# Optimization experiments

Hardware: AMD Instinct MI355X
Metric: run time of the kernel (lower is better)

The kernel has to match this reference:

```python
import jax, jax.numpy as jnp
import numpy as np

N_NODES = 100000
N_EDGES = 1600000
IN_DIM = 64
HID = 128
N_ASSETS = 50
N_GRAPHS = 64


def setup_inputs() -> dict:
    key = jax.random.key(0)
    ks = jax.random.split(key, 12)
    x = jax.random.normal(ks[0], (N_NODES, IN_DIM), dtype=jnp.float32)
    edge_index = jax.random.randint(ks[1], (2, N_EDGES), 0, N_NODES, dtype=jnp.int64)
    batch = jnp.sort(jax.random.randint(ks[2], (N_NODES,), 0, N_GRAPHS, dtype=jnp.int64))
    def lin(k, fan_in, fan_out):
        bound = 1.0 / np.sqrt(fan_in)
        return jax.random.uniform(k, (fan_in, fan_out), jnp.float32, -bound, bound)
    return {
        "x": x,
        "edge_index": edge_index,
        "batch": batch,
        # GraphConv 1: lin_rel (with bias) on aggregated messages, lin_root (no bias)
        "w1_rel": lin(ks[3], IN_DIM, HID),
        "b1": jnp.zeros((HID,), jnp.float32),
        "w1_root": lin(ks[4], IN_DIM, HID),
        # GraphConv 2
        "w2_rel": lin(ks[5], HID, HID),
        "b2": jnp.zeros((HID,), jnp.float32),
        "w2_root": lin(ks[6], HID, HID),
        # MLP head
        "fc1_w": lin(ks[7], HID, HID),
        "fc1_b": jnp.zeros((HID,), jnp.float32),
        "fc2_w": lin(ks[8], HID, N_ASSETS),
        "fc2_b": jnp.zeros((N_ASSETS,), jnp.float32),
    }


def graph_conv(x, src, dst, w_rel, w_root, b):
    # out_i = W_rel @ (sum_{j: j->i} x_j) + W_root @ x_i + b  (PyG GraphConv, aggr='add')
    # Project first (cheaper traffic when out_dim <= in_dim is not guaranteed, but
    # aggregating raw features then projecting matches math; project-then-scatter is
    # equivalent by linearity and lets the scatter run at out width. Keep faithful
    # order: aggregate raw x_j, then lin_rel.
    agg = jax.ops.segment_sum(x[src], dst, num_segments=N_NODES)  # [N, in_dim]
    return agg @ w_rel + x @ w_root + b


def reference(x, edge_index, batch, w1_rel, b1, w1_root, w2_rel, b2, w2_root,
              fc1_w, fc1_b, fc2_w, fc2_b):
    src, dst = edge_index[0], edge_index[1]
    h = jax.nn.relu(graph_conv(x, src, dst, w1_rel, w1_root, b1))   # [N, HID]
    h = jax.nn.relu(graph_conv(h, src, dst, w2_rel, w2_root, b2))   # [N, HID]
    # global_mean_pool over batch segment ids
    sums = jax.ops.segment_sum(h, batch, num_segments=N_GRAPHS)     # [G, HID]
    cnts = jax.ops.segment_sum(jnp.ones((h.shape[0], 1), h.dtype), batch,
                               num_segments=N_GRAPHS)               # [G, 1]
    pooled = sums / jnp.maximum(cnts, 1.0)
    out = jax.nn.relu(pooled @ fc1_w + fc1_b)
    logits = out @ fc2_w + fc2_b
    return jax.nn.softmax(logits, axis=-1)
```

## Files before the change

kernel.cpp:

```cpp
#include <hip/hip_runtime.h>
#include <math.h>

#define N_NODES_C 100000
#define N_EDGES_C 1600000
#define IN_DIM_C 64
#define HID_C 128
#define N_ASSETS_C 50
#define N_GRAPHS_C 64

#define BKT_SHIFT 9
#define BKT_NODES 512
#define NB_BKT ((N_NODES_C + BKT_NODES - 1) / BKT_NODES)
#define EPB_A 8192
#define NBLK_A ((N_EDGES_C + EPB_A - 1) / EPB_A)

typedef __attribute__((ext_vector_type(8))) short bf16x8;
typedef __attribute__((ext_vector_type(4))) float f32x4;

__device__ __forceinline__ unsigned short f2bf(float f) {
    unsigned u = __float_as_uint(f);
    return (unsigned short)((u + 0x7FFFu + ((u >> 16) & 1u)) >> 16);
}
__device__ __forceinline__ float bf2f(unsigned short b) {
    return __uint_as_float((unsigned)b << 16);
}

__global__ __launch_bounds__(256) void cast_bf16_kernel(
    const float* __restrict__ src, unsigned short* __restrict__ dst, int n4)
{
    int i = blockIdx.x * 256 + threadIdx.x;
    if (i < n4) {
        float4 v = ((const float4*)src)[i];
        ushort4 o;
        o.x = f2bf(v.x); o.y = f2bf(v.y); o.z = f2bf(v.z); o.w = f2bf(v.w);
        ((ushort4*)dst)[i] = o;
    }
}

__global__ __launch_bounds__(64) void pack_w_kernel(
    const float* __restrict__ W, unsigned short* __restrict__ dst)
{
    int kc = blockIdx.x >> 3;
    int ct = blockIdx.x & 7;
    int lane = threadIdx.x;
    int quad = lane >> 4;
    int l16 = lane & 15;
    unsigned short hi[8], lo[8];
#pragma unroll
    for (int j = 0; j < 8; ++j) {
        float w = W[(size_t)(kc * 32 + quad * 8 + j) * HID_C + ct * 16 + l16];
        unsigned short h = f2bf(w);
        float r = w - bf2f(h);
        hi[j] = h;
        lo[j] = f2bf(r);
    }
    size_t base = ((size_t)(kc * 8 + ct) * 2) * 512 + (size_t)lane * 8;
#pragma unroll
    for (int j = 0; j < 8; ++j) {
        dst[base + j] = hi[j];
        dst[base + 512 + j] = lo[j];
    }
}

__global__ __launch_bounds__(256) void bucket_hist_kernel(
    const int* __restrict__ ei, int* __restrict__ bcnt)
{
    __shared__ int cnt[NB_BKT];
    int t = threadIdx.x;
    for (int i = t; i < NB_BKT; i += 256) cnt[i] = 0;
    __syncthreads();
    int base = blockIdx.x * 2048;
#pragma unroll
    for (int i = 0; i < 8; ++i) {
        int e = base + i * 256 + t;
        if (e < N_EDGES_C) {
            int dst = ei[N_EDGES_C + e];
            atomicAdd(&cnt[dst >> BKT_SHIFT], 1);
        }
    }
    __syncthreads();
    for (int i = t; i < NB_BKT; i += 256)
        if (cnt[i]) atomicAdd(&bcnt[i], cnt[i]);
}

__global__ __launch_bounds__(256) void bucket_scan_kernel(
    const int* __restrict__ bcnt, int* __restrict__ bbase, int* __restrict__ gcur)
{
    __shared__ int s[256];
    int t = threadIdx.x;
    int v = (t < NB_BKT) ? bcnt[t] : 0;
    s[t] = v;
    __syncthreads();
    for (int o = 1; o < 256; o <<= 1) {
        int x = (t >= o) ? s[t - o] : 0;
        __syncthreads();
        s[t] += x;
        __syncthreads();
    }
    int excl = s[t] - v;
    if (t < NB_BKT) { bbase[t] = excl; gcur[t] = excl; }
    if (t == 255) bbase[NB_BKT] = s[255];
}

__global__ __launch_bounds__(256) void partition_kernel(
    const int* __restrict__ ei, int* __restrict__ gcur,
    unsigned* __restrict__ tmp)
{
    __shared__ unsigned stage[EPB_A];
    __shared__ unsigned stage2[EPB_A];
    __shared__ unsigned char sbkt[EPB_A];
    __shared__ unsigned char sbkt2[EPB_A];
    __shared__ int cnt[NB_BKT];
    __shared__ int base[NB_BKT];
    __shared__ int cur[NB_BKT];
    __shared__ int gb[NB_BKT];
    __shared__ int s[256];

    const int t = threadIdx.x;
    const int e0 = blockIdx.x * EPB_A;
    const int nE = min(EPB_A, N_EDGES_C - e0);

    for (int i = t; i < NB_BKT; i += 256) cnt[i] = 0;
    __syncthreads();

    for (int idx = t; idx < nE; idx += 256) {
        int e = e0 + idx;
        int src = ei[e];
        int dst = ei[N_EDGES_C + e];
        int b = dst >> BKT_SHIFT;
        stage[idx] = ((unsigned)(dst & (BKT_NODES - 1)) << 17) | (unsigned)src;
        sbkt[idx] = (unsigned char)b;
        atomicAdd(&cnt[b], 1);
    }
    __syncthreads();

    int v = (t < NB_BKT) ? cnt[t] : 0;
    s[t] = v;
    __syncthreads();
    for (int o = 1; o < 256; o <<= 1) {
        int x = (t >= o) ? s[t - o] : 0;
        __syncthreads();
        s[t] += x;
        __syncthreads();
    }
    if (t < NB_BKT) {
        int excl = s[t] - v;
        base[t] = excl;
        cur[t] = excl;
        gb[t] = atomicAdd(&gcur[t], v);
    }
    __syncthreads();

    for (int idx = t; idx < nE; idx += 256) {
        int b = sbkt[idx];
        int p = atomicAdd(&cur[b], 1);
        stage2[p] = stage[idx];
        sbkt2[p] = (unsigned char)b;
    }
    __syncthreads();

    for (int idx = t; idx < nE; idx += 256) {
        int b = sbkt2[idx];
        int dest = gb[b] + (idx - base[b]);
        tmp[dest] = stage2[idx];
    }
}

__global__ __launch_bounds__(256) void bucket_sort_kernel(
    const unsigned* __restrict__ tmp, const int* __restrict__ bbase,
    int* __restrict__ row_ptr, int* __restrict__ col)
{
    __shared__ int ldeg[BKT_NODES];
    __shared__ int lsum[256];
    const int t = threadIdx.x;
    const int b = blockIdx.x;
    const int beg = bbase[b];
    const int end = bbase[b + 1];

    ldeg[t] = 0; ldeg[t + 256] = 0;
    __syncthreads();

    for (int p = beg + t; p < end; p += 256)
        atomicAdd(&ldeg[tmp[p] >> 17], 1);
    __syncthreads();

    int a0 = ldeg[2 * t], a1 = ldeg[2 * t + 1];
    int pair = a0 + a1;
    lsum[t] = pair;
    __syncthreads();
    for (int o = 1; o < 256; o <<= 1) {
        int x = (t >= o) ? lsum[t - o] : 0;
        __syncthreads();
        lsum[t] += x;
        __syncthreads();
    }
    int ep = lsum[t] - pair;
    __syncthreads();
    ldeg[2 * t] = ep;
    ldeg[2 * t + 1] = ep + a0;

    int gn0 = b * BKT_NODES + 2 * t;
    if (gn0 < N_NODES_C)     row_ptr[gn0] = beg + ep;
    if (gn0 + 1 < N_NODES_C) row_ptr[gn0 + 1] = beg + ep + a0;
    if (b == NB_BKT - 1 && t == 0) row_ptr[N_NODES_C] = N_EDGES_C;
    __syncthreads();

    for (int p = beg + t; p < end; p += 256) {
        unsigned v = tmp[p];
        int pos = atomicAdd(&ldeg[v >> 17], 1);
        col[beg + pos] = (int)(v & 0x1FFFFu);
    }
}

__global__ __launch_bounds__(256) void gather_bf128_kernel(
    const unsigned short* __restrict__ feat, const int* __restrict__ row_ptr,
    const int* __restrict__ col, unsigned short* __restrict__ agg)
{
    int wave = threadIdx.x >> 6;
    int lane = threadIdx.x & 63;
    int g = lane >> 4;
    int c = lane & 15;
    int n = blockIdx.x * 4 + wave;
    if (n >= N_NODES_C) return;
    int beg = row_ptr[n], end = row_ptr[n + 1];
    const uint4* f4 = (const uint4*)feat;

    float acc[8];
#pragma unroll
    for (int j = 0; j < 8; ++j) acc[j] = 0.f;

    int e = beg + g;
    for (; e + 4 < end; e += 8) {
        int s0 = col[e], s1 = col[e + 4];
        uint4 v0 = f4[(size_t)s0 * 16 + c];
        uint4 v1 = f4[(size_t)s1 * 16 + c];
        acc[0] += __uint_as_float(v0.x << 16) + __uint_as_float(v1.x << 16);
        acc[1] += __uint_as_float(v0.x & 0xFFFF0000u) + __uint_as_float(v1.x & 0xFFFF0000u);
        acc[2] += __uint_as_float(v0.y << 16) + __uint_as_float(v1.y << 16);
        acc[3] += __uint_as_float(v0.y & 0xFFFF0000u) + __uint_as_float(v1.y & 0xFFFF0000u);
        acc[4] += __uint_as_float(v0.z << 16) + __uint_as_float(v1.z << 16);
        acc[5] += __uint_as_float(v0.z & 0xFFFF0000u) + __uint_as_float(v1.z & 0xFFFF0000u);
        acc[6] += __uint_as_float(v0.w << 16) + __uint_as_float(v1.w << 16);
        acc[7] += __uint_as_float(v0.w & 0xFFFF0000u) + __uint_as_float(v1.w & 0xFFFF0000u);
    }
    if (e < end) {
        uint4 v = f4[(size_t)col[e] * 16 + c];
        acc[0] += __uint_as_float(v.x << 16);
        acc[1] += __uint_as_float(v.x & 0xFFFF0000u);
        acc[2] += __uint_as_float(v.y << 16);
        acc[3] += __uint_as_float(v.y & 0xFFFF0000u);
        acc[4] += __uint_as_float(v.z << 16);
        acc[5] += __uint_as_float(v.z & 0xFFFF0000u);
        acc[6] += __uint_as_float(v.w << 16);
        acc[7] += __uint_as_float(v.w & 0xFFFF0000u);
    }
#pragma unroll
    for (int j = 0; j < 8; ++j) {
        acc[j] += __shfl_xor(acc[j], 16, 64);
        acc[j] += __shfl_xor(acc[j], 32, 64);
    }
    if (g == 0) {
        uint4 o;
        o.x = (unsigned)f2bf(acc[0]) | ((unsigned)f2bf(acc[1]) << 16);
        o.y = (unsigned)f2bf(acc[2]) | ((unsigned)f2bf(acc[3]) << 16);
        o.z = (unsigned)f2bf(acc[4]) | ((unsigned)f2bf(acc[5]) << 16);
        o.w = (unsigned)f2bf(acc[6]) | ((unsigned)f2bf(acc[7]) << 16);
        ((uint4*)agg)[(size_t)n * 16 + c] = o;
    }
}

__global__ __launch_bounds__(256) void gather_bf64_kernel(
    const unsigned short* __restrict__ feat, const int* __restrict__ row_ptr,
    const int* __restrict__ col, unsigned short* __restrict__ agg)
{
    int wave = threadIdx.x >> 6;
    int lane = threadIdx.x & 63;
    int g = lane >> 3;
    int c = lane & 7;
    int n = blockIdx.x * 4 + wave;
    if (n >= N_NODES_C) return;
    int beg = row_ptr[n], end = row_ptr[n + 1];
    const uint4* f4 = (const uint4*)feat;

    float acc[8];
#pragma unroll
    for (int j = 0; j < 8; ++j) acc[j] = 0.f;

    int e = beg + g;
    for (; e + 8 < end; e += 16) {
        int s0 = col[e], s1 = col[e + 8];
        uint4 v0 = f4[(size_t)s0 * 8 + c];
        uint4 v1 = f4[(size_t)s1 * 8 + c];
        acc[0] += __uint_as_float(v0.x << 16) + __uint_as_float(v1.x << 16);
        acc[1] += __uint_as_float(v0.x & 0xFFFF0000u) + __uint_as_float(v1.x & 0xFFFF0000u);
        acc[2] += __uint_as_float(v0.y << 16) + __uint_as_float(v1.y << 16);
        acc[3] += __uint_as_float(v0.y & 0xFFFF0000u) + __uint_as_float(v1.y & 0xFFFF0000u);
        acc[4] += __uint_as_float(v0.z << 16) + __uint_as_float(v1.z << 16);
        acc[5] += __uint_as_float(v0.z & 0xFFFF0000u) + __uint_as_float(v1.z & 0xFFFF0000u);
        acc[6] += __uint_as_float(v0.w << 16) + __uint_as_float(v1.w << 16);
        acc[7] += __uint_as_float(v0.w & 0xFFFF0000u) + __uint_as_float(v1.w & 0xFFFF0000u);
    }
    if (e < end) {
        uint4 v = f4[(size_t)col[e] * 8 + c];
        acc[0] += __uint_as_float(v.x << 16);
        acc[1] += __uint_as_float(v.x & 0xFFFF0000u);
        acc[2] += __uint_as_float(v.y << 16);
        acc[3] += __uint_as_float(v.y & 0xFFFF0000u);
        acc[4] += __uint_as_float(v.z << 16);
        acc[5] += __uint_as_float(v.z & 0xFFFF0000u);
        acc[6] += __uint_as_float(v.w << 16);
        acc[7] += __uint_as_float(v.w & 0xFFFF0000u);
    }
#pragma unroll
    for (int j = 0; j < 8; ++j) {
        acc[j] += __shfl_xor(acc[j], 8, 64);
        acc[j] += __shfl_xor(acc[j], 16, 64);
        acc[j] += __shfl_xor(acc[j], 32, 64);
    }
    if (g == 0) {
        uint4 o;
        o.x = (unsigned)f2bf(acc[0]) | ((unsigned)f2bf(acc[1]) << 16);
        o.y = (unsigned)f2bf(acc[2]) | ((unsigned)f2bf(acc[3]) << 16);
        o.z = (unsigned)f2bf(acc[4]) | ((unsigned)f2bf(acc[5]) << 16);
        o.w = (unsigned)f2bf(acc[6]) | ((unsigned)f2bf(acc[7]) << 16);
        ((uint4*)agg)[(size_t)n * 8 + c] = o;
    }
}

template<int K>
__device__ __forceinline__ void conv_phase(
    const unsigned short* __restrict__ P, const unsigned short* __restrict__ WP,
    const int* rowIdx, int quad, int lane, int wv, f32x4 acc[4][2])
{
#pragma unroll
    for (int kc = 0; kc < K / 32; ++kc) {
        bf16x8 afr[4];
#pragma unroll
        for (int rt = 0; rt < 4; ++rt)
            afr[rt] = *(const bf16x8*)(P + (size_t)rowIdx[rt] * K + kc * 32 + quad * 8);
#pragma unroll
        for (int ci = 0; ci < 2; ++ci) {
            int ct = wv * 2 + ci;
            const unsigned short* bp = WP + ((size_t)(kc * 8 + ct) * 2) * 512 + (size_t)lane * 8;
            bf16x8 bhi = *(const bf16x8*)bp;
            bf16x8 blo = *(const bf16x8*)(bp + 512);
#pragma unroll
            for (int rt = 0; rt < 4; ++rt) {
                acc[rt][ci] = __builtin_amdgcn_mfma_f32_16x16x32_bf16(afr[rt], bhi, acc[rt][ci], 0, 0, 0);
                acc[rt][ci] = __builtin_amdgcn_mfma_f32_16x16x32_bf16(afr[rt], blo, acc[rt][ci], 0, 0, 0);
            }
        }
    }
}

template<int KA, int KX, bool OUTF32>
__global__ __launch_bounds__(256) void conv_mfma_kernel(
    const unsigned short* __restrict__ A, const unsigned short* __restrict__ X,
    const unsigned short* __restrict__ WrP, const unsigned short* __restrict__ WoP,
    const float* __restrict__ bias, void* __restrict__ outp, int N)
{
    const int t = threadIdx.x;
    const int wv = t >> 6;
    const int lane = t & 63;
    const int quad = lane >> 4;
    const int l16 = lane & 15;
    const int n0 = blockIdx.x * 64;

    f32x4 acc[4][2];
#pragma unroll
    for (int rt = 0; rt < 4; ++rt)
#pragma unroll
        for (int ci = 0; ci < 2; ++ci)
            acc[rt][ci] = (f32x4){0.f, 0.f, 0.f, 0.f};

    int rowIdx[4];
#pragma unroll
    for (int rt = 0; rt < 4; ++rt) {
        int r = n0 + rt * 16 + l16;
        rowIdx[rt] = (r < N) ? r : (N - 1);
    }

    conv_phase<KA>(A, WrP, rowIdx, quad, lane, wv, acc);
    conv_phase<KX>(X, WoP, rowIdx, quad, lane, wv, acc);

#pragma unroll
    for (int ci = 0; ci < 2; ++ci) {
        int colg = wv * 32 + ci * 16 + l16;
        float bv = bias[colg];
#pragma unroll
        for (int rt = 0; rt < 4; ++rt) {
            int nbase = n0 + rt * 16 + quad * 4;
#pragma unroll
            for (int r = 0; r < 4; ++r) {
                int node = nbase + r;
                if (node < N) {
                    float v = fmaxf(acc[rt][ci][r] + bv, 0.f);
                    if (OUTF32)
                        ((float*)outp)[(size_t)node * HID_C + colg] = v;
                    else
                        ((unsigned short*)outp)[(size_t)node * HID_C + colg] = f2bf(v);
                }
            }
        }
    }
}

__global__ __launch_bounds__(128) void pool_kernel(
    const float* __restrict__ h, const int* __restrict__ batch,
    float* __restrict__ pooled, float* __restrict__ cnts, int N)
{
    int j  = threadIdx.x;
    int n0 = blockIdx.x * 128;
    int nend = min(n0 + 128, N);
    int cur = -1;
    float sum = 0.f, cnt = 0.f;
    for (int n = n0; n < nend; ++n) {
        int g = batch[n];
        if (g != cur) {
            if (cur >= 0) {
                atomicAdd(&pooled[cur * HID_C + j], sum);
                if (j == 0) atomicAdd(&cnts[cur], cnt);
            }
            cur = g; sum = 0.f; cnt = 0.f;
        }
        sum += h[(size_t)n * HID_C + j];
        cnt += 1.f;
    }
    if (cur >= 0) {
        atomicAdd(&pooled[cur * HID_C + j], sum);
        if (j == 0) atomicAdd(&cnts[cur], cnt);
    }
}

__global__ __launch_bounds__(128) void head_kernel(
    const float* __restrict__ pooled, const float* __restrict__ cnts,
    const float* __restrict__ fc1w, const float* __restrict__ fc1b,
    const float* __restrict__ fc2w, const float* __restrict__ fc2b,
    float* __restrict__ out)
{
    __shared__ float sp[HID_C];
    __shared__ float so[HID_C];
    __shared__ float sl[64];
    __shared__ float sred[2];
    int g = blockIdx.x;
    int j = threadIdx.x;

    float inv = 1.f / fmaxf(cnts[g], 1.f);
    sp[j] = pooled[g * HID_C + j] * inv;
    __syncthreads();

    float a = fc1b[j];
    for (int k = 0; k < HID_C; ++k) a = fmaf(sp[k], fc1w[k * HID_C + j], a);
    so[j] = fmaxf(a, 0.f);
    __syncthreads();

    if (j < N_ASSETS_C) {
        float l = fc2b[j];
        for (int k = 0; k < HID_C; ++k) l = fmaf(so[k], fc2w[k * N_ASSETS_C + j], l);
        sl[j] = l;
    }
    __syncthreads();

    if (j == 0) {
        float m = -1e30f;
        for (int q = 0; q < N_ASSETS_C; ++q) m = fmaxf(m, sl[q]);
        sred[0] = m;
    }
    __syncthreads();
    if (j < N_ASSETS_C) sl[j] = expf(sl[j] - sred[0]);
    __syncthreads();
    if (j == 0) {
        float s = 0.f;
        for (int q = 0; q < N_ASSETS_C; ++q) s += sl[q];
        sred[1] = 1.f / s;
    }
    __syncthreads();
    if (j < N_ASSETS_C) out[g * N_ASSETS_C + j] = sl[j] * sred[1];
}

extern "C" void kernel_launch(void* const* d_in, const int* in_sizes, int n_in,
                              void* d_out, int out_size, void* d_ws, size_t ws_size,
                              hipStream_t stream)
{
    const float* x       = (const float*)d_in[0];
    const int*   ei      = (const int*)d_in[1];
    const int*   batch   = (const int*)d_in[2];
    const float* w1_rel  = (const float*)d_in[3];
    const float* b1      = (const float*)d_in[4];
    const float* w1_root = (const float*)d_in[5];
    const float* w2_rel  = (const float*)d_in[6];
    const float* b2      = (const float*)d_in[7];
    const float* w2_root = (const float*)d_in[8];
    const float* fc1w    = (const float*)d_in[9];
    const float* fc1b    = (const float*)d_in[10];
    const float* fc2w    = (const float*)d_in[11];
    const float* fc2b    = (const float*)d_in[12];
    float* out = (float*)d_out;

    char* ws = (char*)d_ws;
    unsigned*       tmp     = (unsigned*)(ws + 0);
    int*            col     = (int*)(ws + 6400000);
    int*            row_ptr = (int*)(ws + 12800000);
    int*            bcnt    = (int*)(ws + 13200016);
    int*            bbase   = (int*)(ws + 13200816);
    int*            gcur    = (int*)(ws + 13201616);
    unsigned short* wp1r    = (unsigned short*)(ws + 13202432);
    unsigned short* wp1o    = (unsigned short*)(ws + 13235200);
    unsigned short* wp2r    = (unsigned short*)(ws + 13267968);
    unsigned short* wp2o    = (unsigned short*)(ws + 13333504);
    float*          pooled  = (float*)(ws + 13399040);
    float*          cnts    = (float*)(ws + 13431808);
    unsigned short* xb      = (unsigned short*)(ws + 13432064);
    unsigned short* agg1b   = (unsigned short*)(ws + 26232064);
    unsigned short* h1b     = (unsigned short*)(ws + 39032064);
    unsigned short* agg2b   = (unsigned short*)(ws + 64632064);
    float*          h2      = (float*)(ws + 90232064);

    hipMemsetAsync(pooled, 0, 33024, stream);
    hipMemsetAsync(bcnt, 0, 800, stream);

    cast_bf16_kernel<<<(N_NODES_C * IN_DIM_C / 4 + 255) / 256, 256, 0, stream>>>(x, xb, N_NODES_C * IN_DIM_C / 4);
    pack_w_kernel<<<(IN_DIM_C / 32) * 8, 64, 0, stream>>>(w1_rel,  wp1r);
    pack_w_kernel<<<(IN_DIM_C / 32) * 8, 64, 0, stream>>>(w1_root, wp1o);
    pack_w_kernel<<<(HID_C  / 32) * 8, 64, 0, stream>>>(w2_rel,  wp2r);
    pack_w_kernel<<<(HID_C  / 32) * 8, 64, 0, stream>>>(w2_root, wp2o);

    bucket_hist_kernel<<<(N_EDGES_C + 2047) / 2048, 256, 0, stream>>>(ei, bcnt);
    bucket_scan_kernel<<<1, 256, 0, stream>>>(bcnt, bbase, gcur);
    partition_kernel<<<NBLK_A, 256, 0, stream>>>(ei, gcur, tmp);
    bucket_sort_kernel<<<NB_BKT, 256, 0, stream>>>(tmp, bbase, row_ptr, col);

    const int ggrid = (N_NODES_C + 3) / 4;
    const int cgrid = (N_NODES_C + 63) / 64;

    gather_bf64_kernel<<<ggrid, 256, 0, stream>>>(xb, row_ptr, col, agg1b);
    conv_mfma_kernel<IN_DIM_C, IN_DIM_C, false><<<cgrid, 256, 0, stream>>>(
        agg1b, xb, wp1r, wp1o, b1, (void*)h1b, N_NODES_C);

    gather_bf128_kernel<<<ggrid, 256, 0, stream>>>(h1b, row_ptr, col, agg2b);
    conv_mfma_kernel<HID_C, HID_C, true><<<cgrid, 256, 0, stream>>>(
        agg2b, h1b, wp2r, wp2o, b2, (void*)h2, N_NODES_C);

    const int pgrid = (N_NODES_C + 127) / 128;
    pool_kernel<<<pgrid, 128, 0, stream>>>(h2, batch, pooled, cnts, N_NODES_C);
    head_kernel<<<N_GRAPHS_C, 128, 0, stream>>>(pooled, cnts, fc1w, fc1b, fc2w, fc2b, out);
}
```

Measured before the change: 394.9 us.

## Fuse mean-pool into second conv epilogue and unroll 128-wide gather

Layer 2's MFMA conv kernel now reduces its ReLU outputs straight into per-graph pooled sums with atomics, using batch ids held in shared memory. This drops the fp32 h2 write, its re-read, and the separate pool kernel. Node counts per graph move to a small standalone count kernel. The 128-wide gather loop is unrolled to four outstanding loads per thread to raise memory-level parallelism, at the cost of more registers and more atomics per block when a tile spans several graphs.

```diff
diff --git a/kernel.cpp b/kernel.cpp
--- a/kernel.cpp
+++ b/kernel.cpp
@@ -23,6 +23,16 @@
 }
 __device__ __forceinline__ float bf2f(unsigned short b) {
     return __uint_as_float((unsigned)b << 16);
+}
+__device__ __forceinline__ void acc_bf8(float* acc, uint4 v) {
+    acc[0] += __uint_as_float(v.x << 16);
+    acc[1] += __uint_as_float(v.x & 0xFFFF0000u);
+    acc[2] += __uint_as_float(v.y << 16);
+    acc[3] += __uint_as_float(v.y & 0xFFFF0000u);
+    acc[4] += __uint_as_float(v.z << 16);
+    acc[5] += __uint_as_float(v.z & 0xFFFF0000u);
+    acc[6] += __uint_as_float(v.w << 16);
+    acc[7] += __uint_as_float(v.w & 0xFFFF0000u);
 }
 
 __global__ __launch_bounds__(256) void cast_bf16_kernel(
@@ -230,29 +240,24 @@
     for (int j = 0; j < 8; ++j) acc[j] = 0.f;
 
     int e = beg + g;
-    for (; e + 4 < end; e += 8) {
+    for (; e + 12 < end; e += 16) {
+        int s0 = col[e], s1 = col[e + 4], s2 = col[e + 8], s3 = col[e + 12];
+        uint4 v0 = f4[(size_t)s0 * 16 + c];
+        uint4 v1 = f4[(size_t)s1 * 16 + c];
+        uint4 v2 = f4[(size_t)s2 * 16 + c];
+        uint4 v3 = f4[(size_t)s3 * 16 + c];
+        acc_bf8(acc, v0); acc_bf8(acc, v1); acc_bf8(acc, v2); acc_bf8(acc, v3);
+    }
+    if (e + 4 < end) {
         int s0 = col[e], s1 = col[e + 4];
         uint4 v0 = f4[(size_t)s0 * 16 + c];
         uint4 v1 = f4[(size_t)s1 * 16 + c];
-        acc[0] += __uint_as_float(v0.x << 16) + __uint_as_float(v1.x << 16);
-        acc[1] += __uint_as_float(v0.x & 0xFFFF0000u) + __uint_as_float(v1.x & 0xFFFF0000u);
-        acc[2] += __uint_as_float(v0.y << 16) + __uint_as_float(v1.y << 16);
-        acc[3] += __uint_as_float(v0.y & 0xFFFF0000u) + __uint_as_float(v1.y & 0xFFFF0000u);
-        acc[4] += __uint_as_float(v0.z << 16) + __uint_as_float(v1.z << 16);
-        acc[5] += __uint_as_float(v0.z & 0xFFFF0000u) + __uint_as_float(v1.z & 0xFFFF0000u);
-        acc[6] += __uint_as_float(v0.w << 16) + __uint_as_float(v1.w << 16);
-        acc[7] += __uint_as_float(v0.w & 0xFFFF0000u) + __uint_as_float(v1.w & 0xFFFF0000u);
+        acc_bf8(acc, v0); acc_bf8(acc, v1);
+        e += 8;
     }
     if (e < end) {
         uint4 v = f4[(size_t)col[e] * 16 + c];
-        acc[0] += __uint_as_float(v.x << 16);
-        acc[1] += __uint_as_float(v.x & 0xFFFF0000u);
-        acc[2] += __uint_as_float(v.y << 16);
-        acc[3] += __uint_as_float(v.y & 0xFFFF0000u);
-        acc[4] += __uint_as_float(v.z << 16);
-        acc[5] += __uint_as_float(v.z & 0xFFFF0000u);
-        acc[6] += __uint_as_float(v.w << 16);
-        acc[7] += __uint_as_float(v.w & 0xFFFF0000u);
+        acc_bf8(acc, v);
     }
 #pragma unroll
     for (int j = 0; j < 8; ++j) {
@@ -291,25 +296,11 @@
         int s0 = col[e], s1 = col[e + 8];
         uint4 v0 = f4[(size_t)s0 * 8 + c];
         uint4 v1 = f4[(size_t)s1 * 8 + c];
-        acc[0] += __uint_as_float(v0.x << 16) + __uint_as_float(v1.x << 16);
-        acc[1] += __uint_as_float(v0.x & 0xFFFF0000u) + __uint_as_float(v1.x & 0xFFFF0000u);
-        acc[2] += __uint_as_float(v0.y << 16) + __uint_as_float(v1.y << 16);
-        acc[3] += __uint_as_float(v0.y & 0xFFFF0000u) + __uint_as_float(v1.y & 0xFFFF0000u);
-        acc[4] += __uint_as_float(v0.z << 16) + __uint_as_float(v1.z << 16);
-        acc[5] += __uint_as_float(v0.z & 0xFFFF0000u) + __uint_as_float(v1.z & 0xFFFF0000u);
-        acc[6] += __uint_as_float(v0.w << 16) + __uint_as_float(v1.w << 16);
-        acc[7] += __uint_as_float(v0.w & 0xFFFF0000u) + __uint_as_float(v1.w & 0xFFFF0000u);
+        acc_bf8(acc, v0); acc_bf8(acc, v1);
     }
     if (e < end) {
         uint4 v = f4[(size_t)col[e] * 8 + c];
-        acc[0] += __uint_as_float(v.x << 16);
-        acc[1] += __uint_as_float(v.x & 0xFFFF0000u);
-        acc[2] += __uint_as_float(v.y << 16);
-        acc[3] += __uint_as_float(v.y & 0xFFFF0000u);
-        acc[4] += __uint_as_float(v.z << 16);
-        acc[5] += __uint_as_float(v.z & 0xFFFF0000u);
-        acc[6] += __uint_as_float(v.w << 16);
-        acc[7] += __uint_as_float(v.w & 0xFFFF0000u);
+        acc_bf8(acc, v);
     }
 #pragma unroll
     for (int j = 0; j < 8; ++j) {
@@ -353,11 +344,11 @@
     }
 }
 
-template<int KA, int KX, bool OUTF32>
+template<int KA, int KX>
 __global__ __launch_bounds__(256) void conv_mfma_kernel(
     const unsigned short* __restrict__ A, const unsigned short* __restrict__ X,
     const unsigned short* __restrict__ WrP, const unsigned short* __restrict__ WoP,
-    const float* __restrict__ bias, void* __restrict__ outp, int N)
+    const float* __restrict__ bias, unsigned short* __restrict__ outp, int N)
 {
     const int t = threadIdx.x;
     const int wv = t >> 6;
@@ -393,43 +384,105 @@
 #pragma unroll
             for (int r = 0; r < 4; ++r) {
                 int node = nbase + r;
-                if (node < N) {
-                    float v = fmaxf(acc[rt][ci][r] + bv, 0.f);
-                    if (OUTF32)
-                        ((float*)outp)[(size_t)node * HID_C + colg] = v;
-                    else
-                        ((unsigned short*)outp)[(size_t)node * HID_C + colg] = f2bf(v);
-                }
+                if (node < N)
+                    outp[(size_t)node * HID_C + colg] = f2bf(fmaxf(acc[rt][ci][r] + bv, 0.f));
             }
         }
     }
 }
 
-__global__ __launch_bounds__(128) void pool_kernel(
-    const float* __restrict__ h, const int* __restrict__ batch,
-    float* __restrict__ pooled, float* __restrict__ cnts, int N)
-{
-    int j  = threadIdx.x;
-    int n0 = blockIdx.x * 128;
-    int nend = min(n0 + 128, N);
-    int cur = -1;
-    float sum = 0.f, cnt = 0.f;
-    for (int n = n0; n < nend; ++n) {
-        int g = batch[n];
-        if (g != cur) {
-            if (cur >= 0) {
-                atomicAdd(&pooled[cur * HID_C + j], sum);
-                if (j == 0) atomicAdd(&cnts[cur], cnt);
+template<int KA, int KX>
+__global__ __launch_bounds__(256) void conv_mfma_pool_kernel(
+    const unsigned short* __restrict__ A, const unsigned short* __restrict__ X,
+    const unsigned short* __restrict__ WrP, const unsigned short* __restrict__ WoP,
+    const float* __restrict__ bias, const int* __restrict__ batch,
+    float* __restrict__ pooled, int N)
+{
+    __shared__ int sbatch[64];
+    const int t = threadIdx.x;
+    const int wv = t >> 6;
+    const int lane = t & 63;
+    const int quad = lane >> 4;
+    const int l16 = lane & 15;
+    const int n0 = blockIdx.x * 64;
+
+    if (t < 64) {
+        int node = n0 + t;
+        sbatch[t] = (node < N) ? batch[node] : -1;
+    }
+
+    f32x4 acc[4][2];
+#pragma unroll
+    for (int rt = 0; rt < 4; ++rt)
+#pragma unroll
+        for (int ci = 0; ci < 2; ++ci)
+            acc[rt][ci] = (f32x4){0.f, 0.f, 0.f, 0.f};
+
+    int rowIdx[4];
+#pragma unroll
+    for (int rt = 0; rt < 4; ++rt) {
+        int r = n0 + rt * 16 + l16;
+        rowIdx[rt] = (r < N) ? r : (N - 1);
+    }
+
+    conv_phase<KA>(A, WrP, rowIdx, quad, lane, wv, acc);
+    conv_phase<KX>(X, WoP, rowIdx, quad, lane, wv, acc);
+    __syncthreads();
+
+#pragma unroll
+    for (int ci = 0; ci < 2; ++ci) {
+        float bv = bias[wv * 32 + ci * 16 + l16];
+#pragma unroll
+        for (int rt = 0; rt < 4; ++rt)
+#pragma unroll
+            for (int r = 0; r < 4; ++r)
+                acc[rt][ci][r] = fmaxf(acc[rt][ci][r] + bv, 0.f);
+    }
+
+    int gmin = sbatch[0];
+    int gmax = batch[min(n0 + 63, N - 1)];
+    for (int gg = gmin; gg <= gmax; ++gg) {
+#pragma unroll
+        for (int ci = 0; ci < 2; ++ci) {
+            float p = 0.f;
+#pragma unroll
+            for (int rt = 0; rt < 4; ++rt) {
+                int lbase = rt * 16 + quad * 4;
+#pragma unroll
+                for (int r = 0; r < 4; ++r)
+                    if (sbatch[lbase + r] == gg) p += acc[rt][ci][r];
             }
-            cur = g; sum = 0.f; cnt = 0.f;
+            p += __shfl_xor(p, 16, 64);
+            p += __shfl_xor(p, 32, 64);
+            if (quad == 0)
+                atomicAdd(&pooled[gg * HID_C + wv * 32 + ci * 16 + l16], p);
         }
-        sum += h[(size_t)n * HID_C + j];
-        cnt += 1.f;
-    }
-    if (cur >= 0) {
-        atomicAdd(&pooled[cur * HID_C + j], sum);
-        if (j == 0) atomicAdd(&cnts[cur], cnt);
-    }
+    }
+}
+
+__global__ __launch_bounds__(256) void count_kernel(
+    const int* __restrict__ batch, float* __restrict__ cnts, int N)
+{
+    __shared__ int h[N_GRAPHS_C];
+    int t = threadIdx.x;
+    if (t < N_GRAPHS_C) h[t] = 0;
+    __syncthreads();
+    int base = (blockIdx.x * 256 + t) * 16;
+    int cur = -1, c = 0;
+    for (int i = 0; i < 16; ++i) {
+        int n = base + i;
+        if (n < N) {
+            int g = batch[n];
+            if (g != cur) {
+                if (cur >= 0) atomicAdd(&h[cur], c);
+                cur = g; c = 0;
+            }
+            ++c;
+        }
+    }
+    if (cur >= 0) atomicAdd(&h[cur], c);
+    __syncthreads();
+    if (t < N_GRAPHS_C && h[t]) atomicAdd(&cnts[t], (float)h[t]);
 }
 
 __global__ __launch_bounds__(128) void head_kernel(
@@ -514,7 +567,6 @@
     unsigned short* agg1b   = (unsigned short*)(ws + 26232064);
     unsigned short* h1b     = (unsigned short*)(ws + 39032064);
     unsigned short* agg2b   = (unsigned short*)(ws + 64632064);
-    float*          h2      = (float*)(ws + 90232064);
 
     hipMemsetAsync(pooled, 0, 33024, stream);
     hipMemsetAsync(bcnt, 0, 800, stream);
@@ -525,6 +577,8 @@
     pack_w_kernel<<<(HID_C  / 32) * 8, 64, 0, stream>>>(w2_rel,  wp2r);
     pack_w_kernel<<<(HID_C  / 32) * 8, 64, 0, stream>>>(w2_root, wp2o);
 
+    count_kernel<<<(N_NODES_C + 4095) / 4096, 256, 0, stream>>>(batch, cnts, N_NODES_C);
+
     bucket_hist_kernel<<<(N_EDGES_C + 2047) / 2048, 256, 0, stream>>>(ei, bcnt);
     bucket_scan_kernel<<<1, 256, 0, stream>>>(bcnt, bbase, gcur);
     partition_kernel<<<NBLK_A, 256, 0, stream>>>(ei, gcur, tmp);
@@ -534,14 +588,12 @@
     const int cgrid = (N_NODES_C + 63) / 64;
 
     gather_bf64_kernel<<<ggrid, 256, 0, stream>>>(xb, row_ptr, col, agg1b);
-    conv_mfma_kernel<IN_DIM_C, IN_DIM_C, false><<<cgrid, 256, 0, stream>>>(
-        agg1b, xb, wp1r, wp1o, b1, (void*)h1b, N_NODES_C);
+    conv_mfma_kernel<IN_DIM_C, IN_DIM_C><<<cgrid, 256, 0, stream>>>(
+        agg1b, xb, wp1r, wp1o, b1, h1b, N_NODES_C);
 
     gather_bf128_kernel<<<ggrid, 256, 0, stream>>>(h1b, row_ptr, col, agg2b);
-    conv_mfma_kernel<HID_C, HID_C, true><<<cgrid, 256, 0, stream>>>(
-        agg2b, h1b, wp2r, wp2o, b2, (void*)h2, N_NODES_C);
-
-    const int pgrid = (N_NODES_C + 127) / 128;
-    pool_kernel<<<pgrid, 128, 0, stream>>>(h2, batch, pooled, cnts, N_NODES_C);
+    conv_mfma_pool_kernel<HID_C, HID_C><<<cgrid, 256, 0, stream>>>(
+        agg2b, h1b, wp2r, wp2o, b2, batch, pooled, N_NODES_C);
+
     head_kernel<<<N_GRAPHS_C, 128, 0, stream>>>(pooled, cnts, fc1w, fc1b, fc2w, fc2b, out);
 }
```

Result: faster. 348.2 us (-11.8%).
